# Performance work log

Hardware: AMD Instinct MI355X
Metric: run time of the kernel (lower is better)

Reference implementation:

```python
import jax, jax.numpy as jnp
import numpy as np

B, CHAR_LEN, LSTM, VOCAB, NATTN = 4096, 64, 400, 73, 10

def _lstm_cell(x, h, c, W_ih, W_hh, b):
    # gates: [B, 4*LSTM] in (i, f, g, o) order, matching torch.nn.LSTMCell
    g = x @ W_ih.T + h @ W_hh.T + b
    i, f, gg, o = jnp.split(g, 4, axis=1)
    i = jax.nn.sigmoid(i); f = jax.nn.sigmoid(f)
    gg = jnp.tanh(gg); o = jax.nn.sigmoid(o)
    c_new = f * c + i * gg
    h_new = o * jnp.tanh(c_new)
    return h_new, c_new

def setup_inputs() -> dict:
    key = jax.random.key(0)
    ks = jax.random.split(key, 24)
    d = {}
    d['inputs'] = jax.random.normal(ks[0], (B, 3), jnp.float32)
    for n, k in zip(['h1','c1','h2','c2','h3','c3'], ks[1:7]):
        d[n] = jax.random.normal(k, (B, LSTM), jnp.float32) * 0.1
    d['kappa'] = jax.random.uniform(ks[7], (B, NATTN), jnp.float32) * 5.0
    d['w_prev'] = jax.random.uniform(ks[8], (B, VOCAB), jnp.float32)
    d['attention_values'] = jax.random.uniform(ks[9], (B, CHAR_LEN, VOCAB), jnp.float32)
    d['attention_lengths'] = jax.random.randint(ks[10], (B,), 1, CHAR_LEN + 1, jnp.int32)
    s = 0.05
    in1 = VOCAB + 3              # lstm1 input: [w, inputs]
    in23 = 3 + LSTM + VOCAB      # lstm2/3 input: [inputs, h, w]
    attn_in = VOCAB + 3 + LSTM
    d['W_ih1'] = jax.random.normal(ks[11], (4 * LSTM, in1), jnp.float32) * s
    d['W_hh1'] = jax.random.normal(ks[12], (4 * LSTM, LSTM), jnp.float32) * s
    d['b1'] = jax.random.normal(ks[13], (4 * LSTM,), jnp.float32) * s
    d['W_attn'] = jax.random.normal(ks[14], (3 * NATTN, attn_in), jnp.float32) * s
    d['b_attn'] = jax.random.normal(ks[15], (3 * NATTN,), jnp.float32) * s
    d['W_ih2'] = jax.random.normal(ks[16], (4 * LSTM, in23), jnp.float32) * s
    d['W_hh2'] = jax.random.normal(ks[17], (4 * LSTM, LSTM), jnp.float32) * s
    d['b2'] = jax.random.normal(ks[18], (4 * LSTM,), jnp.float32) * s
    d['W_ih3'] = jax.random.normal(ks[19], (4 * LSTM, in23), jnp.float32) * s
    d['W_hh3'] = jax.random.normal(ks[20], (4 * LSTM, LSTM), jnp.float32) * s
    d['b3'] = jax.random.normal(ks[21], (4 * LSTM,), jnp.float32) * s
    return d

def reference(inputs, h1, c1, h2, c2, h3, c3, kappa, w_prev, attention_values,
              attention_lengths, W_ih1, W_hh1, b1, W_attn, b_attn,
              W_ih2, W_hh2, b2, W_ih3, W_hh3, b3):
    char_len = attention_values.shape[1]
    # --- LSTM 1 ---
    s1_in = jnp.concatenate([w_prev, inputs], axis=1)
    h1n, c1n = _lstm_cell(s1_in, h1, c1, W_ih1, W_hh1, b1)
    # --- Gaussian-mixture location attention ---
    attn_in = jnp.concatenate([w_prev, inputs, h1n], axis=1)
    attn_params = jax.nn.softplus(attn_in @ W_attn.T + b_attn)
    alpha, beta, kap = jnp.split(attn_params, 3, axis=1)
    kap = kappa + kap / 25.0
    beta = jnp.maximum(beta, 0.01)
    u = jnp.arange(char_len, dtype=jnp.float32)[None, None, :]           # [1,1,C]
    phi = jnp.sum(alpha[:, :, None] *
                  jnp.exp(-jnp.square(kap[:, :, None] - u) / beta[:, :, None]),
                  axis=1)                                                 # [B,C]
    seq_mask = (jnp.arange(char_len)[None, :] < attention_lengths[:, None]).astype(jnp.float32)
    w = jnp.einsum('bc,bcv->bv', phi * seq_mask, attention_values)        # [B,V]
    # --- LSTM 2 & 3 ---
    s2_in = jnp.concatenate([inputs, h1n, w], axis=1)
    h2n, c2n = _lstm_cell(s2_in, h2, c2, W_ih2, W_hh2, b2)
    s3_in = jnp.concatenate([inputs, h2n, w], axis=1)
    h3n, c3n = _lstm_cell(s3_in, h3, c3, W_ih3, W_hh3, b3)
    return h3n
```

## Files before the change

### kernel.cpp

```cpp
#include <hip/hip_runtime.h>
#include <hip/hip_bf16.h>


#define B_SZ     4096
#define LSTM_N   400
#define NG       1600
#define VOCAB    73
#define NATTN    10
#define CHARLEN  64
#define KP1      512
#define KP23     896

typedef _Float16 half8 __attribute__((ext_vector_type(8)));
typedef __attribute__((ext_vector_type(4))) float floatx4;

__device__ __forceinline__ void gload_lds16(const void* g, void* l) {
    __builtin_amdgcn_global_load_lds(
        (const __attribute__((address_space(1))) void*)g,
        (__attribute__((address_space(3))) void*)l, 16, 0, 0);
}

__device__ __forceinline__ int lds_off(int r, int g) {
    return (r << 6) + ((((g ^ r) & 7)) << 3);
}

__global__ __launch_bounds__(256) void pack_wall(const float* __restrict__ Wih1,
                                                 const float* __restrict__ Whh1,
                                                 const float* __restrict__ Wih2,
                                                 const float* __restrict__ Whh2,
                                                 const float* __restrict__ Wih3,
                                                 const float* __restrict__ Whh3,
                                                 const float* __restrict__ W_attn,
                                                 _Float16* __restrict__ W1,
                                                 _Float16* __restrict__ W2,
                                                 _Float16* __restrict__ W3,
                                                 _Float16* __restrict__ Wa)
{
    const int z = blockIdx.z;
    const int n = blockIdx.y;
    const int k = blockIdx.x * 256 + threadIdx.x;
    if (z == 3) {
        if (n >= 64 || k >= KP1) return;
        float v = (n < 30 && k < 476) ? W_attn[(size_t)n * 476 + k] : 0.f;
        Wa[(size_t)n * KP1 + k] = (_Float16)v;
        return;
    }
    if (n >= NG) return;
    const int u = n >> 2, g = n & 3;
    const int src = g * 400 + u;
    if (z == 0) {
        if (k >= KP1) return;
        float v = 0.f;
        if (k < 76)           v = Wih1[(size_t)src * 76 + k];
        else if (k < 476)     v = Whh1[(size_t)src * 400 + (k - 76)];
        W1[(size_t)n * KP1 + k] = (_Float16)v;
    } else {
        if (k >= KP23) return;
        const float* Wih = (z == 1) ? Wih2 : Wih3;
        const float* Whh = (z == 1) ? Whh2 : Whh3;
        float v = 0.f;
        if (k < 476)          v = Wih[(size_t)src * 476 + k];
        else if (k < 876)     v = Whh[(size_t)src * 400 + (k - 476)];
        ((z == 1) ? W2 : W3)[(size_t)n * KP23 + k] = (_Float16)v;
    }
}

__global__ __launch_bounds__(256) void pack_x(const float* __restrict__ w_prev,
                                              const float* __restrict__ inputs,
                                              const float* __restrict__ h1,
                                              const float* __restrict__ h2,
                                              const float* __restrict__ h3,
                                              _Float16* __restrict__ X1,
                                              _Float16* __restrict__ XA,
                                              _Float16* __restrict__ X2,
                                              _Float16* __restrict__ X3)
{
    const int b = blockIdx.y;
    const int k = blockIdx.x * 256 + threadIdx.x;
    if (k < KP1) {
        float v = 0.f;
        if (k < 73)        v = w_prev[(size_t)b * 73 + k];
        else if (k < 76)   v = inputs[(size_t)b * 3 + (k - 73)];
        else if (k < 476)  v = h1[(size_t)b * 400 + (k - 76)];
        X1[(size_t)b * KP1 + k] = (_Float16)v;
        if (k < 76 || k >= 476) XA[(size_t)b * KP1 + k] = (_Float16)v;
    }
    const int kk = k - KP1;
    if (kk >= 0 && kk < KP23) {
        if (kk >= 3 && kk < 476) return;
        float v2 = 0.f, v3 = 0.f;
        if (kk < 3) { v2 = inputs[(size_t)b * 3 + kk]; v3 = v2; }
        else if (kk >= 476 && kk < 876) {
            v2 = h2[(size_t)b * 400 + (kk - 476)];
            v3 = h3[(size_t)b * 400 + (kk - 476)];
        }
        X2[(size_t)b * KP23 + kk] = (_Float16)v2;
        X3[(size_t)b * KP23 + kk] = (_Float16)v3;
    }
}

template<int KP>
__global__ __launch_bounds__(256) void gemm_fused_t(const _Float16* __restrict__ Wm,
                                                    const _Float16* __restrict__ X,
                                                    const float* __restrict__ bias,
                                                    const float* __restrict__ c_in,
                                                    _Float16* __restrict__ d1, int ld1,
                                                    _Float16* __restrict__ d2, int ld2,
                                                    float* __restrict__ fout)
{
    __shared__ _Float16 As[2][64 * 64];
    __shared__ _Float16 Bs[2][128 * 64];

    const int t    = threadIdx.x;
    const int w    = t >> 6;
    const int lane = t & 63;
    const int quad = lane >> 4;
    const int l16  = lane & 15;
    const int m0   = blockIdx.y * 64;
    const int n0   = blockIdx.x * 128;
    const int wm   = (w >> 1) * 32;
    const int wn   = (w & 1) * 64;
    const int lr   = lane >> 3;
    const int gq   = (lane & 7) ^ lr;

    floatx4 acc[2][4] = {};

    auto stage = [&](int sb, int k0) {
        const int cr = w * 16;
#pragma unroll
        for (int s = 0; s < 2; s++)
            gload_lds16(Wm + (size_t)(m0 + cr + s * 8 + lr) * KP + k0 + gq * 8,
                        &As[sb][(cr + s * 8) * 64]);
#pragma unroll
        for (int j = 0; j < 2; j++) {
            const int cr2 = (j * 4 + w) * 16;
#pragma unroll
            for (int s = 0; s < 2; s++)
                gload_lds16(X + (size_t)(n0 + cr2 + s * 8 + lr) * KP + k0 + gq * 8,
                            &Bs[sb][(cr2 + s * 8) * 64]);
        }
    };

    stage(0, 0);
    constexpr int NT = KP / 64;
#pragma unroll
    for (int kt = 0; kt < NT; kt++) {
        const int sb = kt & 1;
        if (kt + 1 < NT) {
            stage(sb ^ 1, (kt + 1) * 64);
            asm volatile("s_waitcnt vmcnt(6)" ::: "memory");
        } else {
            asm volatile("s_waitcnt vmcnt(0)" ::: "memory");
        }
        __builtin_amdgcn_s_barrier();
        __builtin_amdgcn_sched_barrier(0);

#pragma unroll
        for (int h = 0; h < 2; h++) {
            half8 af[2], bf[4];
#pragma unroll
            for (int i = 0; i < 2; i++)
                af[i] = *(const half8*)(&As[sb][lds_off(wm + i * 16 + l16, h * 4 + quad)]);
#pragma unroll
            for (int i = 0; i < 4; i++)
                bf[i] = *(const half8*)(&Bs[sb][lds_off(wn + i * 16 + l16, h * 4 + quad)]);
#pragma unroll
            for (int mt = 0; mt < 2; mt++)
#pragma unroll
                for (int nt = 0; nt < 4; nt++)
                    acc[mt][nt] = __builtin_amdgcn_mfma_f32_16x16x32_f16(
                        af[mt], bf[nt], acc[mt][nt], 0, 0, 0);
        }
        __builtin_amdgcn_s_barrier();
    }

#pragma unroll
    for (int mt = 0; mt < 2; mt++) {
        const int u = ((m0 + wm + mt * 16) >> 2) + quad;
        const float bi  = bias[u];
        const float bff = bias[400 + u];
        const float bg  = bias[800 + u];
        const float bo  = bias[1200 + u];
#pragma unroll
        for (int nt = 0; nt < 4; nt++) {
            const int b = n0 + wn + nt * 16 + l16;
            float gi = acc[mt][nt][0] + bi;
            float gf = acc[mt][nt][1] + bff;
            float gg = acc[mt][nt][2] + bg;
            float go = acc[mt][nt][3] + bo;
            float si = 1.f / (1.f + expf(-gi));
            float sf = 1.f / (1.f + expf(-gf));
            float so = 1.f / (1.f + expf(-go));
            float cn = sf * c_in[(size_t)b * LSTM_N + u] + si * tanhf(gg);
            float h  = so * tanhf(cn);
            if (fout) {
                fout[(size_t)b * LSTM_N + u] = h;
            } else {
                _Float16 hh = (_Float16)h;
                d1[(size_t)b * ld1 + u] = hh;
                if (d2) d2[(size_t)b * ld2 + u] = hh;
            }
        }
    }
}

__global__ __launch_bounds__(256) void gemm_plain(const _Float16* __restrict__ Wa,
                                                  const _Float16* __restrict__ XA,
                                                  const float* __restrict__ bias,
                                                  float* __restrict__ C)
{
    __shared__ _Float16 As[2][64 * 64];
    __shared__ _Float16 Bs[2][128 * 64];

    const int t    = threadIdx.x;
    const int w    = t >> 6;
    const int lane = t & 63;
    const int quad = lane >> 4;
    const int l16  = lane & 15;
    const int n0   = blockIdx.x * 128;
    const int wm   = (w >> 1) * 32;
    const int wn   = (w & 1) * 64;
    const int lr   = lane >> 3;
    const int gq   = (lane & 7) ^ lr;

    floatx4 acc[2][4] = {};

    auto stage = [&](int sb, int k0) {
        const int cr = w * 16;
#pragma unroll
        for (int s = 0; s < 2; s++)
            gload_lds16(Wa + (size_t)(cr + s * 8 + lr) * KP1 + k0 + gq * 8,
                        &As[sb][(cr + s * 8) * 64]);
#pragma unroll
        for (int j = 0; j < 2; j++) {
            const int cr2 = (j * 4 + w) * 16;
#pragma unroll
            for (int s = 0; s < 2; s++)
                gload_lds16(XA + (size_t)(n0 + cr2 + s * 8 + lr) * KP1 + k0 + gq * 8,
                            &Bs[sb][(cr2 + s * 8) * 64]);
        }
    };

    stage(0, 0);
    constexpr int NT = KP1 / 64;
#pragma unroll
    for (int kt = 0; kt < NT; kt++) {
        const int sb = kt & 1;
        if (kt + 1 < NT) {
            stage(sb ^ 1, (kt + 1) * 64);
            asm volatile("s_waitcnt vmcnt(6)" ::: "memory");
        } else {
            asm volatile("s_waitcnt vmcnt(0)" ::: "memory");
        }
        __builtin_amdgcn_s_barrier();
        __builtin_amdgcn_sched_barrier(0);

#pragma unroll
        for (int h = 0; h < 2; h++) {
            half8 af[2], bf[4];
#pragma unroll
            for (int i = 0; i < 2; i++)
                af[i] = *(const half8*)(&As[sb][lds_off(wm + i * 16 + l16, h * 4 + quad)]);
#pragma unroll
            for (int i = 0; i < 4; i++)
                bf[i] = *(const half8*)(&Bs[sb][lds_off(wn + i * 16 + l16, h * 4 + quad)]);
#pragma unroll
            for (int mt = 0; mt < 2; mt++)
#pragma unroll
                for (int nt = 0; nt < 4; nt++)
                    acc[mt][nt] = __builtin_amdgcn_mfma_f32_16x16x32_f16(
                        af[mt], bf[nt], acc[mt][nt], 0, 0, 0);
        }
        __builtin_amdgcn_s_barrier();
    }

#pragma unroll
    for (int mt = 0; mt < 2; mt++) {
#pragma unroll
        for (int r = 0; r < 4; r++) {
            const int m = wm + mt * 16 + quad * 4 + r;
            if (m >= 30) continue;
            const float bv = bias[m];
#pragma unroll
            for (int nt = 0; nt < 4; nt++) {
                const int b = n0 + wn + nt * 16 + l16;
                C[(size_t)b * 32 + m] = acc[mt][nt][r] + bv;
            }
        }
    }
}

__global__ __launch_bounds__(256) void attn_phi(const float* __restrict__ AP,
                                                const float* __restrict__ kappa,
                                                const float* __restrict__ AV,
                                                const int* __restrict__ alen,
                                                _Float16* __restrict__ X2,
                                                _Float16* __restrict__ X3)
{
    __shared__ float prm[4][32];
    __shared__ float phi_s[4][CHARLEN];

    const int t = threadIdx.x;
    const int wave = t >> 6;
    const int lane = t & 63;
    const int b = blockIdx.x * 4 + wave;

    if (lane < 30) {
        float p  = AP[(size_t)b * 32 + lane];
        float sp = (p > 20.f) ? p : log1pf(expf(p));
        float v;
        if (lane < 10)      v = sp;
        else if (lane < 20) v = fmaxf(sp, 0.01f);
        else                v = kappa[(size_t)b * NATTN + (lane - 20)] + sp * (1.f / 25.f);
        prm[wave][lane] = v;
    }
    __syncthreads();

    const int len = alen[b];
    {
        int c = lane;
        float phi = 0.f;
#pragma unroll
        for (int j = 0; j < NATTN; j++) {
            float d = prm[wave][20 + j] - (float)c;
            phi += prm[wave][j] * expf(-d * d / prm[wave][10 + j]);
        }
        phi_s[wave][c] = (c < len) ? phi : 0.f;
    }
    __syncthreads();

    for (int v0 = 0; v0 < VOCAB; v0 += 64) {
        const int v = v0 + lane;
        if (v < VOCAB) {
            const float* avb = AV + (size_t)b * CHARLEN * VOCAB + v;
            float s = 0.f;
            for (int c = 0; c < len; c++)
                s += phi_s[wave][c] * avb[(size_t)c * VOCAB];
            _Float16 wv = (_Float16)s;
            X2[(size_t)b * KP23 + 403 + v] = wv;
            X3[(size_t)b * KP23 + 403 + v] = wv;
        }
    }
}

extern "C" void kernel_launch(void* const* d_in, const int* in_sizes, int n_in,
                              void* d_out, int out_size, void* d_ws, size_t ws_size,
                              hipStream_t stream)
{
    const float* inputs = (const float*)d_in[0];
    const float* h1     = (const float*)d_in[1];
    const float* c1     = (const float*)d_in[2];
    const float* h2     = (const float*)d_in[3];
    const float* c2     = (const float*)d_in[4];
    const float* h3     = (const float*)d_in[5];
    const float* c3     = (const float*)d_in[6];
    const float* kappa  = (const float*)d_in[7];
    const float* w_prev = (const float*)d_in[8];
    const float* AV     = (const float*)d_in[9];
    const int*   alen   = (const int*)d_in[10];
    const float* W_ih1  = (const float*)d_in[11];
    const float* W_hh1  = (const float*)d_in[12];
    const float* b1     = (const float*)d_in[13];
    const float* W_attn = (const float*)d_in[14];
    const float* b_attn = (const float*)d_in[15];
    const float* W_ih2  = (const float*)d_in[16];
    const float* W_hh2  = (const float*)d_in[17];
    const float* b2     = (const float*)d_in[18];
    const float* W_ih3  = (const float*)d_in[19];
    const float* W_hh3  = (const float*)d_in[20];
    const float* b3     = (const float*)d_in[21];
    float* out = (float*)d_out;

    char* p = (char*)d_ws;
    _Float16* X1 = (_Float16*)p; p += (size_t)B_SZ * KP1 * 2;
    _Float16* XA = (_Float16*)p; p += (size_t)B_SZ * KP1 * 2;
    _Float16* X2 = (_Float16*)p; p += (size_t)B_SZ * KP23 * 2;
    _Float16* X3 = (_Float16*)p; p += (size_t)B_SZ * KP23 * 2;
    _Float16* W1 = (_Float16*)p; p += (size_t)NG * KP1 * 2;
    _Float16* W2 = (_Float16*)p; p += (size_t)NG * KP23 * 2;
    _Float16* W3 = (_Float16*)p; p += (size_t)NG * KP23 * 2;
    _Float16* Wa = (_Float16*)p; p += (size_t)64 * KP1 * 2;
    float* AP = (float*)p;

    pack_wall<<<dim3(4, NG, 4), 256, 0, stream>>>(W_ih1, W_hh1, W_ih2, W_hh2,
                                                  W_ih3, W_hh3, W_attn,
                                                  W1, W2, W3, Wa);
    pack_x<<<dim3((KP1 + KP23 + 255) / 256, B_SZ), 256, 0, stream>>>(
        w_prev, inputs, h1, h2, h3, X1, XA, X2, X3);

    const dim3 fgrid(B_SZ / 128, NG / 64);

    gemm_fused_t<KP1><<<fgrid, 256, 0, stream>>>(W1, X1, b1, c1,
                                                 XA + 76, KP1, X2 + 3, KP23, nullptr);
    gemm_plain<<<dim3(B_SZ / 128, 1), 256, 0, stream>>>(Wa, XA, b_attn, AP);
    attn_phi<<<B_SZ / 4, 256, 0, stream>>>(AP, kappa, AV, alen, X2, X3);
    gemm_fused_t<KP23><<<fgrid, 256, 0, stream>>>(W2, X2, b2, c2,
                                                  X3 + 3, KP23, nullptr, 0, nullptr);
    gemm_fused_t<KP23><<<fgrid, 256, 0, stream>>>(W3, X3, b3, c3,
                                                  nullptr, 0, nullptr, 0, out);
}
```

Before: 309.8 us.

## Merge packing kernels, fuse attention GEMM into phi, stage LSTM epilogue through LDS

The weight and activation packing kernels become one vectorized kernel that writes 8 fp16 values per thread. The packed layouts are reordered so h sits at offset 0, which gives 16-byte aligned epilogue stores. The small attention projection GEMM is folded into the phi kernel as an LDS-staged dot product with wave reductions, removing one launch and the AP round trip. The LSTM epilogue now loads c via vectorized LDS staging and writes h as coalesced vector stores, and s_setprio is raised around the MFMA block. These changes cut launch count and uncoalesced scalar global traffic. The trade-off is extra LDS use and more complex index remapping.

```diff
diff --git a/kernel.cpp b/kernel.cpp
--- a/kernel.cpp
+++ b/kernel.cpp
@@ -24,78 +24,139 @@
     return (r << 6) + ((((g ^ r) & 7)) << 3);
 }
 
-__global__ __launch_bounds__(256) void pack_wall(const float* __restrict__ Wih1,
-                                                 const float* __restrict__ Whh1,
-                                                 const float* __restrict__ Wih2,
-                                                 const float* __restrict__ Whh2,
-                                                 const float* __restrict__ Wih3,
-                                                 const float* __restrict__ Whh3,
-                                                 const float* __restrict__ W_attn,
-                                                 _Float16* __restrict__ W1,
-                                                 _Float16* __restrict__ W2,
-                                                 _Float16* __restrict__ W3,
-                                                 _Float16* __restrict__ Wa)
+#define CW1   102400
+#define CW23  179200
+#define CWA   4096
+#define CX1   262144
+#define CXA   57344
+#define CX23  253952
+#define O1    (CW1)
+#define O2    (O1 + CW23)
+#define O3    (O2 + CW23)
+#define O4    (O3 + CWA)
+#define O5    (O4 + CX1)
+#define O6    (O5 + CXA)
+#define O7    (O6 + CX23)
+
+__global__ __launch_bounds__(256) void pack_all(const float* __restrict__ Wih1,
+                                                const float* __restrict__ Whh1,
+                                                const float* __restrict__ Wih2,
+                                                const float* __restrict__ Whh2,
+                                                const float* __restrict__ Wih3,
+                                                const float* __restrict__ Whh3,
+                                                const float* __restrict__ W_attn,
+                                                const float* __restrict__ w_prev,
+                                                const float* __restrict__ inputs,
+                                                const float* __restrict__ h1,
+                                                const float* __restrict__ h2,
+                                                const float* __restrict__ h3,
+                                                _Float16* __restrict__ W1,
+                                                _Float16* __restrict__ W2,
+                                                _Float16* __restrict__ W3,
+                                                _Float16* __restrict__ Wa,
+                                                _Float16* __restrict__ X1,
+                                                _Float16* __restrict__ XA,
+                                                _Float16* __restrict__ X2,
+                                                _Float16* __restrict__ X3)
 {
-    const int z = blockIdx.z;
-    const int n = blockIdx.y;
-    const int k = blockIdx.x * 256 + threadIdx.x;
-    if (z == 3) {
-        if (n >= 64 || k >= KP1) return;
-        float v = (n < 30 && k < 476) ? W_attn[(size_t)n * 476 + k] : 0.f;
-        Wa[(size_t)n * KP1 + k] = (_Float16)v;
-        return;
-    }
-    if (n >= NG) return;
-    const int u = n >> 2, g = n & 3;
-    const int src = g * 400 + u;
-    if (z == 0) {
-        if (k >= KP1) return;
-        float v = 0.f;
-        if (k < 76)           v = Wih1[(size_t)src * 76 + k];
-        else if (k < 476)     v = Whh1[(size_t)src * 400 + (k - 76)];
-        W1[(size_t)n * KP1 + k] = (_Float16)v;
-    } else {
-        if (k >= KP23) return;
-        const float* Wih = (z == 1) ? Wih2 : Wih3;
-        const float* Whh = (z == 1) ? Whh2 : Whh3;
-        float v = 0.f;
-        if (k < 476)          v = Wih[(size_t)src * 476 + k];
-        else if (k < 876)     v = Whh[(size_t)src * 400 + (k - 476)];
-        ((z == 1) ? W2 : W3)[(size_t)n * KP23 + k] = (_Float16)v;
-    }
-}
-
-__global__ __launch_bounds__(256) void pack_x(const float* __restrict__ w_prev,
-                                              const float* __restrict__ inputs,
-                                              const float* __restrict__ h1,
-                                              const float* __restrict__ h2,
-                                              const float* __restrict__ h3,
-                                              _Float16* __restrict__ X1,
-                                              _Float16* __restrict__ XA,
-                                              _Float16* __restrict__ X2,
-                                              _Float16* __restrict__ X3)
-{
-    const int b = blockIdx.y;
-    const int k = blockIdx.x * 256 + threadIdx.x;
-    if (k < KP1) {
-        float v = 0.f;
-        if (k < 73)        v = w_prev[(size_t)b * 73 + k];
-        else if (k < 76)   v = inputs[(size_t)b * 3 + (k - 73)];
-        else if (k < 476)  v = h1[(size_t)b * 400 + (k - 76)];
-        X1[(size_t)b * KP1 + k] = (_Float16)v;
-        if (k < 76 || k >= 476) XA[(size_t)b * KP1 + k] = (_Float16)v;
-    }
-    const int kk = k - KP1;
-    if (kk >= 0 && kk < KP23) {
-        if (kk >= 3 && kk < 476) return;
-        float v2 = 0.f, v3 = 0.f;
-        if (kk < 3) { v2 = inputs[(size_t)b * 3 + kk]; v3 = v2; }
-        else if (kk >= 476 && kk < 876) {
-            v2 = h2[(size_t)b * 400 + (kk - 476)];
-            v3 = h3[(size_t)b * 400 + (kk - 476)];
-        }
-        X2[(size_t)b * KP23 + kk] = (_Float16)v2;
-        X3[(size_t)b * KP23 + kk] = (_Float16)v3;
+    const int id = blockIdx.x * 256 + threadIdx.x;
+    half8 hv;
+
+    if (id < O1) {
+        const int row = id >> 6;
+        const int k0  = (id & 63) << 3;
+        const int u = row >> 2, g = row & 3;
+        const int src = g * 400 + u;
+#pragma unroll
+        for (int e = 0; e < 8; e++) {
+            const int k = k0 + e;
+            float x = 0.f;
+            if (k < 76)           x = Wih1[(size_t)src * 76 + k];
+            else if (k < 476)     x = Whh1[(size_t)src * 400 + (k - 76)];
+            hv[e] = (_Float16)x;
+        }
+        *(half8*)(W1 + (size_t)row * KP1 + k0) = hv;
+    } else if (id < O3) {
+        const int id2 = id - O1;
+        const bool is3 = (id2 >= CW23);
+        const int id3 = is3 ? id2 - CW23 : id2;
+        const int row = id3 / 112;
+        const int k0  = (id3 - row * 112) << 3;
+        const int u = row >> 2, g = row & 3;
+        const int src = g * 400 + u;
+        const float* Wih = is3 ? Wih3 : Wih2;
+        const float* Whh = is3 ? Whh3 : Whh2;
+#pragma unroll
+        for (int e = 0; e < 8; e++) {
+            const int k = k0 + e;
+            float x = 0.f;
+            if (k < 400)          x = Wih[(size_t)src * 476 + 3 + k];
+            else if (k < 403)     x = Wih[(size_t)src * 476 + (k - 400)];
+            else if (k < 476)     x = Wih[(size_t)src * 476 + k];
+            else if (k < 876)     x = Whh[(size_t)src * 400 + (k - 476)];
+            hv[e] = (_Float16)x;
+        }
+        *(half8*)((is3 ? W3 : W2) + (size_t)row * KP23 + k0) = hv;
+    } else if (id < O4) {
+        const int id4 = id - O3;
+        const int row = id4 >> 6;
+        const int k0  = (id4 & 63) << 3;
+#pragma unroll
+        for (int e = 0; e < 8; e++) {
+            const int k = k0 + e;
+            float x = 0.f;
+            if (row < 30) {
+                if (k < 400)      x = W_attn[(size_t)row * 476 + 76 + k];
+                else if (k < 473) x = W_attn[(size_t)row * 476 + (k - 400)];
+                else if (k < 476) x = W_attn[(size_t)row * 476 + 73 + (k - 473)];
+            }
+            hv[e] = (_Float16)x;
+        }
+        *(half8*)(Wa + (size_t)row * KP1 + k0) = hv;
+    } else if (id < O5) {
+        const int id5 = id - O4;
+        const int b  = id5 >> 6;
+        const int k0 = (id5 & 63) << 3;
+#pragma unroll
+        for (int e = 0; e < 8; e++) {
+            const int k = k0 + e;
+            float x = 0.f;
+            if (k < 73)           x = w_prev[(size_t)b * 73 + k];
+            else if (k < 76)      x = inputs[(size_t)b * 3 + (k - 73)];
+            else if (k < 476)     x = h1[(size_t)b * 400 + (k - 76)];
+            hv[e] = (_Float16)x;
+        }
+        *(half8*)(X1 + (size_t)b * KP1 + k0) = hv;
+    } else if (id < O6) {
+        const int id6 = id - O5;
+        const int b  = id6 / 14;
+        const int k0 = 400 + ((id6 - b * 14) << 3);
+#pragma unroll
+        for (int e = 0; e < 8; e++) {
+            const int k = k0 + e;
+            float x = 0.f;
+            if (k < 473)          x = w_prev[(size_t)b * 73 + (k - 400)];
+            else if (k < 476)     x = inputs[(size_t)b * 3 + (k - 473)];
+            hv[e] = (_Float16)x;
+        }
+        *(half8*)(XA + (size_t)b * KP1 + k0) = hv;
+    } else if (id < O7) {
+        const int id7 = id - O6;
+        const int b  = id7 / 62;
+        const int k0 = 400 + ((id7 - b * 62) << 3);
+        half8 h2v, h3v;
+#pragma unroll
+        for (int e = 0; e < 8; e++) {
+            const int k = k0 + e;
+            float x2 = 0.f, x3 = 0.f;
+            if (k < 403)                    { x2 = inputs[(size_t)b * 3 + (k - 400)]; x3 = x2; }
+            else if (k >= 476 && k < 876)   { x2 = h2[(size_t)b * 400 + (k - 476)];
+                                              x3 = h3[(size_t)b * 400 + (k - 476)]; }
+            h2v[e] = (_Float16)x2;
+            h3v[e] = (_Float16)x3;
+        }
+        *(half8*)(X2 + (size_t)b * KP23 + k0) = h2v;
+        *(half8*)(X3 + (size_t)b * KP23 + k0) = h3v;
     }
 }
 
@@ -164,26 +225,46 @@
 #pragma unroll
             for (int i = 0; i < 4; i++)
                 bf[i] = *(const half8*)(&Bs[sb][lds_off(wn + i * 16 + l16, h * 4 + quad)]);
+            __builtin_amdgcn_s_setprio(1);
 #pragma unroll
             for (int mt = 0; mt < 2; mt++)
 #pragma unroll
                 for (int nt = 0; nt < 4; nt++)
                     acc[mt][nt] = __builtin_amdgcn_mfma_f32_16x16x32_f16(
                         af[mt], bf[nt], acc[mt][nt], 0, 0, 0);
+            __builtin_amdgcn_s_setprio(0);
         }
         __builtin_amdgcn_s_barrier();
     }
+    __builtin_amdgcn_sched_barrier(0);
+
+    const int u0 = m0 >> 2;
+    float*    Cs   = (float*)(&Bs[0][0]);
+    _Float16* Hs16 = (_Float16*)(&As[0][0]);
+    float*    Hs32 = (float*)(&As[0][0]);
+    {
+        const int bl = t >> 1;
+        const int j0 = (t & 1) * 2;
+#pragma unroll
+        for (int j = 0; j < 2; j++) {
+            floatx4 cv = *(const floatx4*)(c_in + (size_t)(n0 + bl) * LSTM_N
+                                           + u0 + (j0 + j) * 4);
+            *(floatx4*)(Cs + bl * 20 + (j0 + j) * 4) = cv;
+        }
+    }
+    __syncthreads();
 
 #pragma unroll
     for (int mt = 0; mt < 2; mt++) {
-        const int u = ((m0 + wm + mt * 16) >> 2) + quad;
+        const int ul = (wm >> 2) + mt * 4 + quad;
+        const int u  = u0 + ul;
         const float bi  = bias[u];
         const float bff = bias[400 + u];
         const float bg  = bias[800 + u];
         const float bo  = bias[1200 + u];
 #pragma unroll
         for (int nt = 0; nt < 4; nt++) {
-            const int b = n0 + wn + nt * 16 + l16;
+            const int bl = wn + nt * 16 + l16;
             float gi = acc[mt][nt][0] + bi;
             float gf = acc[mt][nt][1] + bff;
             float gg = acc[mt][nt][2] + bg;
@@ -191,122 +272,79 @@
             float si = 1.f / (1.f + expf(-gi));
             float sf = 1.f / (1.f + expf(-gf));
             float so = 1.f / (1.f + expf(-go));
-            float cn = sf * c_in[(size_t)b * LSTM_N + u] + si * tanhf(gg);
+            float cn = sf * Cs[bl * 20 + ul] + si * tanhf(gg);
             float h  = so * tanhf(cn);
-            if (fout) {
-                fout[(size_t)b * LSTM_N + u] = h;
-            } else {
-                _Float16 hh = (_Float16)h;
-                d1[(size_t)b * ld1 + u] = hh;
-                if (d2) d2[(size_t)b * ld2 + u] = hh;
-            }
-        }
-    }
-}
-
-__global__ __launch_bounds__(256) void gemm_plain(const _Float16* __restrict__ Wa,
+            if (fout) Hs32[bl * 20 + ul] = h;
+            else      Hs16[bl * 24 + ul] = (_Float16)h;
+        }
+    }
+    __syncthreads();
+
+    if (fout) {
+        const int bl = t >> 1;
+        const int p0 = (t & 1) * 2;
+#pragma unroll
+        for (int j = 0; j < 2; j++) {
+            floatx4 hvv = *(const floatx4*)(Hs32 + bl * 20 + (p0 + j) * 4);
+            *(floatx4*)(fout + (size_t)(n0 + bl) * LSTM_N + u0 + (p0 + j) * 4) = hvv;
+        }
+    } else {
+        const int bl = t >> 1;
+        const int p  = t & 1;
+        half8 hvv = *(const half8*)(Hs16 + bl * 24 + p * 8);
+        *(half8*)(d1 + (size_t)(n0 + bl) * ld1 + u0 + p * 8) = hvv;
+        if (d2) *(half8*)(d2 + (size_t)(n0 + bl) * ld2 + u0 + p * 8) = hvv;
+    }
+}
+
+__global__ __launch_bounds__(256) void attn_fused(const _Float16* __restrict__ Wa,
                                                   const _Float16* __restrict__ XA,
-                                                  const float* __restrict__ bias,
-                                                  float* __restrict__ C)
+                                                  const float* __restrict__ b_attn,
+                                                  const float* __restrict__ kappa,
+                                                  const float* __restrict__ AV,
+                                                  const int* __restrict__ alen,
+                                                  _Float16* __restrict__ X2,
+                                                  _Float16* __restrict__ X3)
 {
-    __shared__ _Float16 As[2][64 * 64];
-    __shared__ _Float16 Bs[2][128 * 64];
-
-    const int t    = threadIdx.x;
-    const int w    = t >> 6;
-    const int lane = t & 63;
-    const int quad = lane >> 4;
-    const int l16  = lane & 15;
-    const int n0   = blockIdx.x * 128;
-    const int wm   = (w >> 1) * 32;
-    const int wn   = (w & 1) * 64;
-    const int lr   = lane >> 3;
-    const int gq   = (lane & 7) ^ lr;
-
-    floatx4 acc[2][4] = {};
-
-    auto stage = [&](int sb, int k0) {
-        const int cr = w * 16;
-#pragma unroll
-        for (int s = 0; s < 2; s++)
-            gload_lds16(Wa + (size_t)(cr + s * 8 + lr) * KP1 + k0 + gq * 8,
-                        &As[sb][(cr + s * 8) * 64]);
-#pragma unroll
-        for (int j = 0; j < 2; j++) {
-            const int cr2 = (j * 4 + w) * 16;
-#pragma unroll
-            for (int s = 0; s < 2; s++)
-                gload_lds16(XA + (size_t)(n0 + cr2 + s * 8 + lr) * KP1 + k0 + gq * 8,
-                            &Bs[sb][(cr2 + s * 8) * 64]);
-        }
-    };
-
-    stage(0, 0);
-    constexpr int NT = KP1 / 64;
-#pragma unroll
-    for (int kt = 0; kt < NT; kt++) {
-        const int sb = kt & 1;
-        if (kt + 1 < NT) {
-            stage(sb ^ 1, (kt + 1) * 64);
-            asm volatile("s_waitcnt vmcnt(6)" ::: "memory");
-        } else {
-            asm volatile("s_waitcnt vmcnt(0)" ::: "memory");
-        }
-        __builtin_amdgcn_s_barrier();
-        __builtin_amdgcn_sched_barrier(0);
-
-#pragma unroll
-        for (int h = 0; h < 2; h++) {
-            half8 af[2], bf[4];
-#pragma unroll
-            for (int i = 0; i < 2; i++)
-                af[i] = *(const half8*)(&As[sb][lds_off(wm + i * 16 + l16, h * 4 + quad)]);
-#pragma unroll
-            for (int i = 0; i < 4; i++)
-                bf[i] = *(const half8*)(&Bs[sb][lds_off(wn + i * 16 + l16, h * 4 + quad)]);
-#pragma unroll
-            for (int mt = 0; mt < 2; mt++)
-#pragma unroll
-                for (int nt = 0; nt < 4; nt++)
-                    acc[mt][nt] = __builtin_amdgcn_mfma_f32_16x16x32_f16(
-                        af[mt], bf[nt], acc[mt][nt], 0, 0, 0);
-        }
-        __builtin_amdgcn_s_barrier();
-    }
-
-#pragma unroll
-    for (int mt = 0; mt < 2; mt++) {
-#pragma unroll
-        for (int r = 0; r < 4; r++) {
-            const int m = wm + mt * 16 + quad * 4 + r;
-            if (m >= 30) continue;
-            const float bv = bias[m];
-#pragma unroll
-            for (int nt = 0; nt < 4; nt++) {
-                const int b = n0 + wn + nt * 16 + l16;
-                C[(size_t)b * 32 + m] = acc[mt][nt][r] + bv;
-            }
-        }
-    }
-}
-
-__global__ __launch_bounds__(256) void attn_phi(const float* __restrict__ AP,
-                                                const float* __restrict__ kappa,
-                                                const float* __restrict__ AV,
-                                                const int* __restrict__ alen,
-                                                _Float16* __restrict__ X2,
-                                                _Float16* __restrict__ X3)
-{
+    __shared__ _Float16 Wa_s[30 * KP1];
     __shared__ float prm[4][32];
     __shared__ float phi_s[4][CHARLEN];
 
     const int t = threadIdx.x;
+#pragma unroll
+    for (int i = 0; i < 8; i++) {
+        const int idx = t + i * 256;
+        if (idx < 1920) {
+            const int row = idx >> 6;
+            const int c8  = (idx & 63) << 3;
+            *(half8*)(&Wa_s[row * KP1 + c8]) = *(const half8*)(Wa + (size_t)row * KP1 + c8);
+        }
+    }
+    __syncthreads();
+
     const int wave = t >> 6;
     const int lane = t & 63;
     const int b = blockIdx.x * 4 + wave;
 
+    half8 xa = *(const half8*)(XA + (size_t)b * KP1 + lane * 8);
+    float xf[8];
+#pragma unroll
+    for (int e = 0; e < 8; e++) xf[e] = (float)xa[e];
+
+    float myp = 0.f;
+#pragma unroll
+    for (int m = 0; m < 30; m++) {
+        half8 wv = *(const half8*)(&Wa_s[m * KP1 + lane * 8]);
+        float s = 0.f;
+#pragma unroll
+        for (int e = 0; e < 8; e++) s += (float)wv[e] * xf[e];
+#pragma unroll
+        for (int sh = 32; sh >= 1; sh >>= 1) s += __shfl_xor(s, sh, 64);
+        if (lane == m) myp = s;
+    }
+
     if (lane < 30) {
-        float p  = AP[(size_t)b * 32 + lane];
+        float p  = myp + b_attn[lane];
         float sp = (p > 20.f) ? p : log1pf(expf(p));
         float v;
         if (lane < 10)      v = sp;
@@ -380,22 +418,19 @@
     _Float16* W2 = (_Float16*)p; p += (size_t)NG * KP23 * 2;
     _Float16* W3 = (_Float16*)p; p += (size_t)NG * KP23 * 2;
     _Float16* Wa = (_Float16*)p; p += (size_t)64 * KP1 * 2;
-    float* AP = (float*)p;
-
-    pack_wall<<<dim3(4, NG, 4), 256, 0, stream>>>(W_ih1, W_hh1, W_ih2, W_hh2,
-                                                  W_ih3, W_hh3, W_attn,
-                                                  W1, W2, W3, Wa);
-    pack_x<<<dim3((KP1 + KP23 + 255) / 256, B_SZ), 256, 0, stream>>>(
-        w_prev, inputs, h1, h2, h3, X1, XA, X2, X3);
+
+    pack_all<<<O7 / 256, 256, 0, stream>>>(W_ih1, W_hh1, W_ih2, W_hh2,
+                                           W_ih3, W_hh3, W_attn,
+                                           w_prev, inputs, h1, h2, h3,
+                                           W1, W2, W3, Wa, X1, XA, X2, X3);
 
     const dim3 fgrid(B_SZ / 128, NG / 64);
 
     gemm_fused_t<KP1><<<fgrid, 256, 0, stream>>>(W1, X1, b1, c1,
-                                                 XA + 76, KP1, X2 + 3, KP23, nullptr);
-    gemm_plain<<<dim3(B_SZ / 128, 1), 256, 0, stream>>>(Wa, XA, b_attn, AP);
-    attn_phi<<<B_SZ / 4, 256, 0, stream>>>(AP, kappa, AV, alen, X2, X3);
+                                                 XA, KP1, X2, KP23, nullptr);
+    attn_fused<<<B_SZ / 4, 256, 0, stream>>>(Wa, XA, b_attn, kappa, AV, alen, X2, X3);
     gemm_fused_t<KP23><<<fgrid, 256, 0, stream>>>(W2, X2, b2, c2,
-                                                  X3 + 3, KP23, nullptr, 0, nullptr);
+                                                  X3, KP23, nullptr, 0, nullptr);
     gemm_fused_t<KP23><<<fgrid, 256, 0, stream>>>(W3, X3, b3, c3,
                                                   nullptr, 0, nullptr, 0, out);
 }
```

Measured after the change: 298.9 us. 3.5% less time.
